# Kernel optimization log

Hardware: AMD Instinct MI355X
Metric: run time of the kernel (lower is better)

The kernel has to match this reference:

```python
import jax, jax.numpy as jnp
import numpy as np

B, D = 64, 65536   # batch, num default boxes
NEG_POS = 3        # negative:positive mining ratio (init arg)


def _bce_with_logits(x, t):
    # numerically stable elementwise BCE-with-logits (matches torch)
    return jnp.maximum(x, 0.0) - x * t + jnp.log1p(jnp.exp(-jnp.abs(x)))


def _smooth_l1(d):
    ad = jnp.abs(d)
    return jnp.where(ad < 1.0, 0.5 * d * d, ad - 0.5)


def setup_inputs() -> dict:
    key = jax.random.key(0)
    k1, k2, k3, k4 = jax.random.split(key, 4)
    loc_data = jax.random.normal(k1, (B, D, 4), dtype=jnp.float32)
    conf_data = jax.random.normal(k2, (B, D, 1), dtype=jnp.float32)
    loc_t = jax.random.normal(k3, (B, D, 4), dtype=jnp.float32)
    conf_t = (jax.random.uniform(k4, (B, D)) < 0.02).astype(jnp.int32)
    return {"loc_data": loc_data, "conf_data": conf_data,
            "loc_t": loc_t, "conf_t": conf_t}


def reference(loc_data, conf_data, loc_t, conf_t):
    pos = conf_t > 0                                  # [B, D]
    num_pos = pos.sum(axis=1, keepdims=True)          # [B, 1]

    # ---- localization loss: smooth-L1 mean over positive box coords ----
    pf = pos[:, :, None].astype(loc_data.dtype)       # [B, D, 1]
    sl1 = _smooth_l1(loc_data - loc_t) * pf           # [B, D, 4]
    n_loc_elems = pf.sum() * 4.0                      # masked-gather -> mean
    loss_l = sl1.sum() / n_loc_elems

    # ---- confidence loss with hard negative mining ----
    logits = conf_data[:, :, 0]                       # [B, D]
    bce = _bce_with_logits(logits, conf_t.astype(logits.dtype))
    bce_neg = jnp.where(pos, 0.0, bce)                # zero-out positives
    # double argsort -> per-row rank of each element's loss (descending)
    loss_idx = jnp.argsort(-bce_neg, axis=1)          # [B, D]
    idx_rank = jnp.argsort(loss_idx, axis=1)          # [B, D]
    num_neg = jnp.minimum(num_pos * NEG_POS, D)       # [B, 1]
    neg = idx_rank < num_neg                          # top-k hardest negatives
    sel = (pos | neg).astype(logits.dtype)            # [B, D]
    loss_c = (bce * sel).sum() / sel.sum()            # mean over selected

    N = num_pos.sum().astype(logits.dtype)
    return (loss_l / N, loss_c / N)
```

## Files before the change

kernel.cpp:

```cpp
#include <hip/hip_runtime.h>
#include <stdint.h>


#define B_ 64
#define D_ 65536
#define NEGPOS 3
#define BPR 16
#define NBLK (B_ * BPR)
#define CHUNK (D_ / BPR)
#define XC 1.25f
#define LCAP 8192
#define HBINS 4096
#define XRANGE 5.0f
#define CJCAP 1024

#define OFF_SL1P     0
#define OFF_BCEP     8192
#define OFF_NP       16384
#define OFF_CC       20480
#define OFF_NEGSUM   24576
#define OFF_KSEL     25088
#define OFF_CAND     32768

__device__ __forceinline__ float softplus_f(float x) {
    return fmaxf(x, 0.0f) + log1pf(expf(-fabsf(x)));
}

__device__ __forceinline__ int bin_of_x(float x) {
    int b = (int)((x - XC) * ((float)HBINS / XRANGE));
    return max(0, min(HBINS - 1, b));
}

__device__ __forceinline__ float smooth_l1_4(float4 a, float4 b) {
    float s = 0.0f, d, ad;
    d = a.x - b.x; ad = fabsf(d); s += (ad < 1.0f) ? 0.5f * d * d : ad - 0.5f;
    d = a.y - b.y; ad = fabsf(d); s += (ad < 1.0f) ? 0.5f * d * d : ad - 0.5f;
    d = a.z - b.z; ad = fabsf(d); s += (ad < 1.0f) ? 0.5f * d * d : ad - 0.5f;
    d = a.w - b.w; ad = fabsf(d); s += (ad < 1.0f) ? 0.5f * d * d : ad - 0.5f;
    return s;
}

__device__ __forceinline__ double wredD(double v) {
#pragma unroll
    for (int o = 32; o > 0; o >>= 1) v += __shfl_down(v, o, 64);
    return v;
}
__device__ __forceinline__ int wredI(int v) {
#pragma unroll
    for (int o = 32; o > 0; o >>= 1) v += __shfl_down(v, o, 64);
    return v;
}

__global__ void __launch_bounds__(256)
mbl_k1(const float4* __restrict__ loc4, const float* __restrict__ conf,
       const float4* __restrict__ loct4, const int* __restrict__ conft,
       unsigned char* __restrict__ ws)
{
    __shared__ float lcand[CHUNK];
    __shared__ unsigned short lpos[CHUNK];
    __shared__ unsigned wtot[4];
    __shared__ double wr[8];

    const int block = blockIdx.x;
    const int base = block * CHUNK;
    const float4* c4 = (const float4*)(conf + base);
    const int4*   t4 = (const int4*)(conft + base);
    const int lane = threadIdx.x & 63, wid = threadIdx.x >> 6;

    float4 xv[4]; int4 tv[4];
#pragma unroll
    for (int it = 0; it < 4; it++) {
        const int g = threadIdx.x + it * 256;
        xv[it] = c4[g];
        tv[it] = t4[g];
    }

    double bcep = 0.0;
    unsigned cntc = 0, cntp = 0;
#pragma unroll
    for (int it = 0; it < 4; it++) {
#pragma unroll
        for (int c = 0; c < 4; c++) {
            float x = (c == 0) ? xv[it].x : (c == 1) ? xv[it].y : (c == 2) ? xv[it].z : xv[it].w;
            int   t = (c == 0) ? tv[it].x : (c == 1) ? tv[it].y : (c == 2) ? tv[it].z : tv[it].w;
            if (t > 0) { cntp++; bcep += (double)(softplus_f(x) - x); }
            else if (x >= XC) cntc++;
        }
    }

    unsigned pk = (cntc << 16) | cntp;
    unsigned incl = pk;
#pragma unroll
    for (int o = 1; o < 64; o <<= 1) {
        unsigned v = __shfl_up(incl, o, 64);
        if (lane >= o) incl += v;
    }
    unsigned excl = incl - pk;
    if (lane == 63) wtot[wid] = incl;
    __syncthreads();
    unsigned wbase = 0;
    for (int w = 0; w < wid; w++) wbase += wtot[w];
    const unsigned tot = wtot[0] + wtot[1] + wtot[2] + wtot[3];
    const unsigned totc = tot >> 16, totp = tot & 0xFFFFu;
    unsigned offc = (excl >> 16) + (wbase >> 16);
    unsigned offp = (excl & 0xFFFFu) + (wbase & 0xFFFFu);

#pragma unroll
    for (int it = 0; it < 4; it++) {
#pragma unroll
        for (int c = 0; c < 4; c++) {
            float x = (c == 0) ? xv[it].x : (c == 1) ? xv[it].y : (c == 2) ? xv[it].z : xv[it].w;
            int   t = (c == 0) ? tv[it].x : (c == 1) ? tv[it].y : (c == 2) ? tv[it].z : tv[it].w;
            const int li = (threadIdx.x + it * 256) * 4 + c;
            if (t > 0) lpos[offp++] = (unsigned short)li;
            else if (x >= XC) lcand[offc++] = x;
        }
    }
    __syncthreads();

    float* seg = (float*)(ws + OFF_CAND) + (size_t)block * CHUNK;
    for (unsigned i = threadIdx.x; i < totc; i += 256) seg[i] = lcand[i];

    double sl1 = 0.0;
    for (unsigned i = threadIdx.x; i < totp; i += 256) {
        const int e = base + (int)lpos[i];
        sl1 += (double)smooth_l1_4(loc4[e], loct4[e]);
    }

    double s1 = wredD(sl1), s2 = wredD(bcep);
    if (lane == 0) { wr[wid] = s1; wr[4 + wid] = s2; }
    __syncthreads();
    if (threadIdx.x == 0) {
        ((double*)(ws + OFF_SL1P))[block] = wr[0] + wr[1] + wr[2] + wr[3];
        ((double*)(ws + OFF_BCEP))[block] = wr[4] + wr[5] + wr[6] + wr[7];
        ((unsigned*)(ws + OFF_NP))[block] = totp;
        ((unsigned*)(ws + OFF_CC))[block] = totc;
    }
}

__device__ __forceinline__ int blockSumI(int v, int* sh) {
    int w = wredI(v);
    const int lane = threadIdx.x & 63, wid = threadIdx.x >> 6;
    __syncthreads();
    if (lane == 0) sh[wid] = w;
    __syncthreads();
    return sh[0] + sh[1] + sh[2] + sh[3];
}

__global__ void __launch_bounds__(256)
mbl_ksel(const float* __restrict__ conf, const int* __restrict__ conft,
         unsigned char* __restrict__ ws)
{
    __shared__ float lval[LCAP];
    __shared__ unsigned hist[HBINS];
    __shared__ unsigned part[256];
    __shared__ unsigned ubuf[CJCAP];
    __shared__ unsigned segoff[BPR + 1];
    __shared__ unsigned scc[BPR];
    __shared__ unsigned wsuf[4];
    __shared__ unsigned shJ, shRemJ, shCj, shNP;
    __shared__ float shXT;
    __shared__ int shI[4];
    __shared__ double wr[4];

    const int row = blockIdx.x;
    const unsigned* cc = (const unsigned*)(ws + OFF_CC) + row * BPR;
    const unsigned* npb = (const unsigned*)(ws + OFF_NP) + row * BPR;
    const int lane = threadIdx.x & 63, wid = threadIdx.x >> 6;

    if (wid == 0) {
        unsigned c = (lane < BPR) ? cc[lane] : 0u;
        unsigned p = (lane < BPR) ? npb[lane] : 0u;
        unsigned inc = c;
#pragma unroll
        for (int o = 1; o < BPR; o <<= 1) {
            unsigned v = __shfl_up(inc, o, 64);
            if (lane >= o) inc += v;
        }
        unsigned ptot = p;
#pragma unroll
        for (int o = 1; o < BPR; o <<= 1) ptot += __shfl_down(ptot, o, 64);
        if (lane < BPR) { segoff[lane] = inc - c; scc[lane] = c; }
        if (lane == BPR - 1) segoff[BPR] = inc;
        if (lane == 0) { shNP = ptot; shCj = 0; }
    }
    __syncthreads();

    const int np = (int)shNP;
    const unsigned n = segoff[BPR];
    long long k = (long long)np * NEGPOS;
    if (k > D_) k = D_;
    long long negs = (long long)D_ - np;
    if (k > negs) k = negs;
    if (threadIdx.x == 0) ((int*)(ws + OFF_KSEL))[row] = (int)k;
    if (k <= 0) {
        if (threadIdx.x == 0) ((double*)(ws + OFF_NEGSUM))[row] = 0.0;
        return;
    }

    const float* cand = (const float*)(ws + OFF_CAND);
    const float* rowc = conf + row * D_;
    const int*   rowt = conft + row * D_;
    const bool fb = ((long long)n < k) || (n > (unsigned)LCAP);
    float xT;
    int rem;

    if (!fb) {
        {
            const int s = threadIdx.x >> 4, li = threadIdx.x & 15;
            const float* gseg = cand + (size_t)(row * BPR + s) * CHUNK;
            const unsigned cs = scc[s], d0 = segoff[s];
            for (unsigned i = li; i < cs; i += 16) lval[d0 + i] = gseg[i];
        }
        for (int i = threadIdx.x; i < HBINS; i += 256) hist[i] = 0;
        __syncthreads();
        for (unsigned i = threadIdx.x; i < n; i += 256)
            atomicAdd(&hist[bin_of_x(lval[i])], 1u);
        __syncthreads();

        {
            unsigned s = 0; const int b0 = threadIdx.x * 16;
#pragma unroll
            for (int i = 0; i < 16; i++) s += hist[b0 + i];
            part[threadIdx.x] = s;
            unsigned suf = s;
#pragma unroll
            for (int o = 1; o < 64; o <<= 1) {
                unsigned v = __shfl_down(suf, o, 64);
                if (lane + o < 64) suf += v;
            }
            if (lane == 0) wsuf[wid] = suf;
            __syncthreads();
            unsigned add = 0;
            for (int w = wid + 1; w < 4; w++) add += wsuf[w];
            suf += add;
            const unsigned sufx = suf - s;
            if ((long long)sufx < k && (long long)suf >= k) {
                long long cum = sufx;
                for (int b = threadIdx.x * 16 + 15; b >= threadIdx.x * 16; b--) {
                    cum += hist[b];
                    if (cum >= k) {
                        shJ = (unsigned)b;
                        shRemJ = (unsigned)(k - (cum - (long long)hist[b]));
                        break;
                    }
                }
            }
        }
        __syncthreads();
        const unsigned J = shJ, remJ = shRemJ;

        for (unsigned i = threadIdx.x; i < n; i += 256) {
            float x = lval[i];
            if ((unsigned)bin_of_x(x) == J) {
                unsigned p = atomicAdd(&shCj, 1u);
                if (p < CJCAP) ubuf[p] = __float_as_uint(x);
            }
        }
        __syncthreads();
        const unsigned cj = shCj;

        if (cj <= CJCAP) {
            for (unsigned i = threadIdx.x; i < cj; i += 256) {
                const float xi = __uint_as_float(ubuf[i]);
                unsigned gt = 0, ge = 0;
                for (unsigned l = 0; l < cj; l++) {
                    const float xl = __uint_as_float(ubuf[l]);
                    gt += (xl > xi) ? 1u : 0u;
                    ge += (xl >= xi) ? 1u : 0u;
                }
                if (gt < remJ && ge >= remJ) shXT = xi;
            }
            __syncthreads();
            xT = shXT;
        } else {
            float flo = XC - 1.0f, fhi = XC + XRANGE + 1.0f;
            for (int it = 0; it < 40; it++) {
                const float mid = 0.5f * (flo + fhi);
                int c = 0;
                for (unsigned i = threadIdx.x; i < n; i += 256)
                    if (lval[i] > mid) c++;
                const int tot = blockSumI(c, shI);
                if ((long long)tot >= k) flo = mid; else fhi = mid;
                if (!(flo < fhi)) break;
            }
            xT = fhi;
        }

        int c = 0;
        double acc = 0.0;
        for (unsigned i = threadIdx.x; i < n; i += 256) {
            float x = lval[i];
            if (x > xT) { c++; acc += (double)softplus_f(x); }
        }
        const int tot = blockSumI(c, shI);
        rem = (int)(k - (long long)tot);
        double t = wredD(acc);
        if (lane == 0) wr[wid] = t;
        __syncthreads();
        if (threadIdx.x == 0)
            ((double*)(ws + OFF_NEGSUM))[row] =
                wr[0] + wr[1] + wr[2] + wr[3] +
                (double)rem * (double)softplus_f(xT);
    } else {
        unsigned lo = 0u, hi = 0xFFFFFFFFu;
        for (int it = 0; it < 32; it++) {
            const unsigned mid = lo + ((hi - lo) >> 1);
            unsigned um = (mid & 0x80000000u) ? (mid & 0x7FFFFFFFu) : ~mid;
            float fm = __uint_as_float(um);
            int c = 0;
            for (int i = threadIdx.x; i < D_; i += 256)
                if (rowt[i] <= 0 && rowc[i] > fm) c++;
            const int tot = blockSumI(c, shI);
            if ((long long)tot >= k) lo = mid; else hi = mid;
        }
        unsigned uT = (hi & 0x80000000u) ? (hi & 0x7FFFFFFFu) : ~hi;
        xT = __uint_as_float(uT);
        int c = 0;
        double acc = 0.0;
        for (int i = threadIdx.x; i < D_; i += 256) {
            if (rowt[i] <= 0) {
                float x = rowc[i];
                if (x > xT) { c++; acc += (double)softplus_f(x); }
            }
        }
        rem = (int)(k - (long long)blockSumI(c, shI));
        double t = wredD(acc);
        if (lane == 0) wr[wid] = t;
        __syncthreads();
        if (threadIdx.x == 0)
            ((double*)(ws + OFF_NEGSUM))[row] =
                wr[0] + wr[1] + wr[2] + wr[3] +
                (double)rem * (double)softplus_f(xT);
    }
}

__global__ void __launch_bounds__(256)
mbl_k5(unsigned char* __restrict__ ws, float* __restrict__ out)
{
    __shared__ double wrA[4], wrB[4], wrC[4];
    __shared__ int shN[4], shK[4];
    const double* sl1p = (const double*)(ws + OFF_SL1P);
    const double* bcep = (const double*)(ws + OFF_BCEP);
    const unsigned* npb = (const unsigned*)(ws + OFF_NP);
    const int* ksel = (const int*)(ws + OFF_KSEL);
    const double* ns = (const double*)(ws + OFF_NEGSUM);

    double a = 0.0, b = 0.0, c = 0.0;
    int n = 0, kk = 0;
    for (int i = threadIdx.x; i < NBLK; i += 256) {
        a += sl1p[i]; b += bcep[i]; n += (int)npb[i];
    }
    if (threadIdx.x < 64) { kk = ksel[threadIdx.x]; c = ns[threadIdx.x]; }

    double ra = wredD(a), rb = wredD(b), rc = wredD(c);
    int rn = wredI(n), rk = wredI(kk);
    const int lane = threadIdx.x & 63, wid = threadIdx.x >> 6;
    if (lane == 0) { wrA[wid] = ra; wrB[wid] = rb; wrC[wid] = rc; shN[wid] = rn; shK[wid] = rk; }
    __syncthreads();
    if (threadIdx.x == 0) {
        double SL1 = wrA[0] + wrA[1] + wrA[2] + wrA[3];
        double BCE = wrB[0] + wrB[1] + wrB[2] + wrB[3];
        double NSUM = wrC[0] + wrC[1] + wrC[2] + wrC[3];
        double Np = (double)(shN[0] + shN[1] + shN[2] + shN[3]);
        double Kt = (double)(shK[0] + shK[1] + shK[2] + shK[3]);
        double out0 = (Np > 0.0) ? (SL1 / (4.0 * Np)) / Np : 0.0;
        double denom = Np + Kt;
        double out1 = (Np > 0.0 && denom > 0.0) ? ((BCE + NSUM) / denom) / Np : 0.0;
        out[0] = (float)out0;
        out[1] = (float)out1;
    }
}

extern "C" void kernel_launch(void* const* d_in, const int* in_sizes, int n_in,
                              void* d_out, int out_size, void* d_ws, size_t ws_size,
                              hipStream_t stream)
{
    const float4* loc4  = (const float4*)d_in[0];
    const float*  conf  = (const float*)d_in[1];
    const float4* loct4 = (const float4*)d_in[2];
    const int*    conft = (const int*)d_in[3];
    unsigned char* ws = (unsigned char*)d_ws;
    float* out = (float*)d_out;

    mbl_k1<<<dim3(NBLK), dim3(256), 0, stream>>>(loc4, conf, loct4, conft, ws);
    mbl_ksel<<<dim3(B_), dim3(256), 0, stream>>>(conf, conft, ws);
    mbl_k5<<<dim3(1), dim3(256), 0, stream>>>(ws, out);
}
```

Baseline: 175.5 us.

## Fuse three kernels into one using last-block-done atomic counters

Merges the per-chunk scan kernel, the per-row hard-negative selection kernel and the final reduction kernel into a single launch. The last block to finish each row, detected through an agent-scope atomic counter, performs that row's selection, and the last row to finish writes the final outputs. Selection now reads candidates straight from global memory instead of staging them in shared memory, and it sums the top-k softplus values directly instead of first locating an exact threshold. This removes two launches and the gaps between them, at the cost of an added memset launch, a serialized tail inside the fused kernel, and a larger shared-memory footprint from the union.

```diff
diff --git a/kernel.cpp b/kernel.cpp
--- a/kernel.cpp
+++ b/kernel.cpp
@@ -9,7 +9,6 @@
 #define NBLK (B_ * BPR)
 #define CHUNK (D_ / BPR)
 #define XC 1.25f
-#define LCAP 8192
 #define HBINS 4096
 #define XRANGE 5.0f
 #define CJCAP 1024
@@ -20,6 +19,7 @@
 #define OFF_CC       20480
 #define OFF_NEGSUM   24576
 #define OFF_KSEL     25088
+#define OFF_CNT      25344
 #define OFF_CAND     32768
 
 __device__ __forceinline__ float softplus_f(float x) {
@@ -51,93 +51,6 @@
     return v;
 }
 
-__global__ void __launch_bounds__(256)
-mbl_k1(const float4* __restrict__ loc4, const float* __restrict__ conf,
-       const float4* __restrict__ loct4, const int* __restrict__ conft,
-       unsigned char* __restrict__ ws)
-{
-    __shared__ float lcand[CHUNK];
-    __shared__ unsigned short lpos[CHUNK];
-    __shared__ unsigned wtot[4];
-    __shared__ double wr[8];
-
-    const int block = blockIdx.x;
-    const int base = block * CHUNK;
-    const float4* c4 = (const float4*)(conf + base);
-    const int4*   t4 = (const int4*)(conft + base);
-    const int lane = threadIdx.x & 63, wid = threadIdx.x >> 6;
-
-    float4 xv[4]; int4 tv[4];
-#pragma unroll
-    for (int it = 0; it < 4; it++) {
-        const int g = threadIdx.x + it * 256;
-        xv[it] = c4[g];
-        tv[it] = t4[g];
-    }
-
-    double bcep = 0.0;
-    unsigned cntc = 0, cntp = 0;
-#pragma unroll
-    for (int it = 0; it < 4; it++) {
-#pragma unroll
-        for (int c = 0; c < 4; c++) {
-            float x = (c == 0) ? xv[it].x : (c == 1) ? xv[it].y : (c == 2) ? xv[it].z : xv[it].w;
-            int   t = (c == 0) ? tv[it].x : (c == 1) ? tv[it].y : (c == 2) ? tv[it].z : tv[it].w;
-            if (t > 0) { cntp++; bcep += (double)(softplus_f(x) - x); }
-            else if (x >= XC) cntc++;
-        }
-    }
-
-    unsigned pk = (cntc << 16) | cntp;
-    unsigned incl = pk;
-#pragma unroll
-    for (int o = 1; o < 64; o <<= 1) {
-        unsigned v = __shfl_up(incl, o, 64);
-        if (lane >= o) incl += v;
-    }
-    unsigned excl = incl - pk;
-    if (lane == 63) wtot[wid] = incl;
-    __syncthreads();
-    unsigned wbase = 0;
-    for (int w = 0; w < wid; w++) wbase += wtot[w];
-    const unsigned tot = wtot[0] + wtot[1] + wtot[2] + wtot[3];
-    const unsigned totc = tot >> 16, totp = tot & 0xFFFFu;
-    unsigned offc = (excl >> 16) + (wbase >> 16);
-    unsigned offp = (excl & 0xFFFFu) + (wbase & 0xFFFFu);
-
-#pragma unroll
-    for (int it = 0; it < 4; it++) {
-#pragma unroll
-        for (int c = 0; c < 4; c++) {
-            float x = (c == 0) ? xv[it].x : (c == 1) ? xv[it].y : (c == 2) ? xv[it].z : xv[it].w;
-            int   t = (c == 0) ? tv[it].x : (c == 1) ? tv[it].y : (c == 2) ? tv[it].z : tv[it].w;
-            const int li = (threadIdx.x + it * 256) * 4 + c;
-            if (t > 0) lpos[offp++] = (unsigned short)li;
-            else if (x >= XC) lcand[offc++] = x;
-        }
-    }
-    __syncthreads();
-
-    float* seg = (float*)(ws + OFF_CAND) + (size_t)block * CHUNK;
-    for (unsigned i = threadIdx.x; i < totc; i += 256) seg[i] = lcand[i];
-
-    double sl1 = 0.0;
-    for (unsigned i = threadIdx.x; i < totp; i += 256) {
-        const int e = base + (int)lpos[i];
-        sl1 += (double)smooth_l1_4(loc4[e], loct4[e]);
-    }
-
-    double s1 = wredD(sl1), s2 = wredD(bcep);
-    if (lane == 0) { wr[wid] = s1; wr[4 + wid] = s2; }
-    __syncthreads();
-    if (threadIdx.x == 0) {
-        ((double*)(ws + OFF_SL1P))[block] = wr[0] + wr[1] + wr[2] + wr[3];
-        ((double*)(ws + OFF_BCEP))[block] = wr[4] + wr[5] + wr[6] + wr[7];
-        ((unsigned*)(ws + OFF_NP))[block] = totp;
-        ((unsigned*)(ws + OFF_CC))[block] = totc;
-    }
-}
-
 __device__ __forceinline__ int blockSumI(int v, int* sh) {
     int w = wredI(v);
     const int lane = threadIdx.x & 63, wid = threadIdx.x >> 6;
@@ -148,29 +61,119 @@
 }
 
 __global__ void __launch_bounds__(256)
-mbl_ksel(const float* __restrict__ conf, const int* __restrict__ conft,
-         unsigned char* __restrict__ ws)
+mbl_fused(const float4* __restrict__ loc4, const float* __restrict__ conf,
+          const float4* __restrict__ loct4, const int* __restrict__ conft,
+          unsigned char* __restrict__ ws, float* __restrict__ out)
 {
-    __shared__ float lval[LCAP];
-    __shared__ unsigned hist[HBINS];
-    __shared__ unsigned part[256];
-    __shared__ unsigned ubuf[CJCAP];
-    __shared__ unsigned segoff[BPR + 1];
-    __shared__ unsigned scc[BPR];
-    __shared__ unsigned wsuf[4];
+    __shared__ union {
+        struct { float lcand[CHUNK]; unsigned short lpos[CHUNK]; } a;
+        struct { unsigned hist[HBINS]; float ubuf[CJCAP]; } b;
+    } u;
+    __shared__ unsigned wtot[4];
+    __shared__ double wr[8];
+    __shared__ double wrC[4];
+    __shared__ int shN[4], shK[4];
+    __shared__ unsigned segoff[BPR + 1], sccS[BPR], wsuf[4];
     __shared__ unsigned shJ, shRemJ, shCj, shNP;
-    __shared__ float shXT;
     __shared__ int shI[4];
-    __shared__ double wr[4];
-
-    const int row = blockIdx.x;
-    const unsigned* cc = (const unsigned*)(ws + OFF_CC) + row * BPR;
-    const unsigned* npb = (const unsigned*)(ws + OFF_NP) + row * BPR;
+    __shared__ int shLast;
+
+    const int block = blockIdx.x;
+    const int row = block >> 4;
+    const int base = block * CHUNK;
     const int lane = threadIdx.x & 63, wid = threadIdx.x >> 6;
 
+    {
+        const float4* c4 = (const float4*)(conf + base);
+        const int4*   t4 = (const int4*)(conft + base);
+
+        float4 xv[4]; int4 tv[4];
+#pragma unroll
+        for (int it = 0; it < 4; it++) {
+            const int g = threadIdx.x + it * 256;
+            xv[it] = c4[g];
+            tv[it] = t4[g];
+        }
+
+        double bcp = 0.0;
+        unsigned cntc = 0, cntp = 0;
+#pragma unroll
+        for (int it = 0; it < 4; it++) {
+#pragma unroll
+            for (int c = 0; c < 4; c++) {
+                float x = (c == 0) ? xv[it].x : (c == 1) ? xv[it].y : (c == 2) ? xv[it].z : xv[it].w;
+                int   t = (c == 0) ? tv[it].x : (c == 1) ? tv[it].y : (c == 2) ? tv[it].z : tv[it].w;
+                if (t > 0) { cntp++; bcp += (double)(softplus_f(x) - x); }
+                else if (x >= XC) cntc++;
+            }
+        }
+
+        unsigned pk = (cntc << 16) | cntp;
+        unsigned incl = pk;
+#pragma unroll
+        for (int o = 1; o < 64; o <<= 1) {
+            unsigned v = __shfl_up(incl, o, 64);
+            if (lane >= o) incl += v;
+        }
+        unsigned excl = incl - pk;
+        if (lane == 63) wtot[wid] = incl;
+        __syncthreads();
+        unsigned wbase = 0;
+        for (int w = 0; w < wid; w++) wbase += wtot[w];
+        const unsigned tot = wtot[0] + wtot[1] + wtot[2] + wtot[3];
+        const unsigned totc = tot >> 16, totp = tot & 0xFFFFu;
+        unsigned offc = (excl >> 16) + (wbase >> 16);
+        unsigned offp = (excl & 0xFFFFu) + (wbase & 0xFFFFu);
+
+#pragma unroll
+        for (int it = 0; it < 4; it++) {
+#pragma unroll
+            for (int c = 0; c < 4; c++) {
+                float x = (c == 0) ? xv[it].x : (c == 1) ? xv[it].y : (c == 2) ? xv[it].z : xv[it].w;
+                int   t = (c == 0) ? tv[it].x : (c == 1) ? tv[it].y : (c == 2) ? tv[it].z : tv[it].w;
+                const int li = (threadIdx.x + it * 256) * 4 + c;
+                if (t > 0) u.a.lpos[offp++] = (unsigned short)li;
+                else if (x >= XC) u.a.lcand[offc++] = x;
+            }
+        }
+        __syncthreads();
+
+        float* seg = (float*)(ws + OFF_CAND) + (size_t)block * CHUNK;
+        for (unsigned i = threadIdx.x; i < totc; i += 256) seg[i] = u.a.lcand[i];
+
+        double sl1 = 0.0;
+        for (unsigned i = threadIdx.x; i < totp; i += 256) {
+            const int e = base + (int)u.a.lpos[i];
+            sl1 += (double)smooth_l1_4(loc4[e], loct4[e]);
+        }
+
+        double s1 = wredD(sl1), s2 = wredD(bcp);
+        if (lane == 0) { wr[wid] = s1; wr[4 + wid] = s2; }
+        __syncthreads();
+        if (threadIdx.x == 0) {
+            ((double*)(ws + OFF_SL1P))[block] = wr[0] + wr[1] + wr[2] + wr[3];
+            ((double*)(ws + OFF_BCEP))[block] = wr[4] + wr[5] + wr[6] + wr[7];
+            ((unsigned*)(ws + OFF_NP))[block] = totp;
+            ((unsigned*)(ws + OFF_CC))[block] = totc;
+        }
+    }
+
+    __syncthreads();
+    if (threadIdx.x == 0) {
+        unsigned old = __hip_atomic_fetch_add(
+            (unsigned*)(ws + OFF_CNT) + row, 1u,
+            __ATOMIC_ACQ_REL, __HIP_MEMORY_SCOPE_AGENT);
+        shLast = (old == BPR - 1) ? 1 : 0;
+    }
+    __syncthreads();
+    if (!shLast) return;
+
+    const unsigned* ccp = (const unsigned*)(ws + OFF_CC) + row * BPR;
+    const unsigned* npp = (const unsigned*)(ws + OFF_NP) + row * BPR;
+
     if (wid == 0) {
-        unsigned c = (lane < BPR) ? cc[lane] : 0u;
-        unsigned p = (lane < BPR) ? npb[lane] : 0u;
+        unsigned c = (lane < BPR) ? ccp[lane] : 0u;
+        unsigned p = (lane < BPR) ? npp[lane] : 0u;
         unsigned inc = c;
 #pragma unroll
         for (int o = 1; o < BPR; o <<= 1) {
@@ -180,7 +183,7 @@
         unsigned ptot = p;
 #pragma unroll
         for (int o = 1; o < BPR; o <<= 1) ptot += __shfl_down(ptot, o, 64);
-        if (lane < BPR) { segoff[lane] = inc - c; scc[lane] = c; }
+        if (lane < BPR) { segoff[lane] = inc - c; sccS[lane] = c; }
         if (lane == BPR - 1) segoff[BPR] = inc;
         if (lane == 0) { shNP = ptot; shCj = 0; }
     }
@@ -193,37 +196,33 @@
     long long negs = (long long)D_ - np;
     if (k > negs) k = negs;
     if (threadIdx.x == 0) ((int*)(ws + OFF_KSEL))[row] = (int)k;
+
+    bool donesum = false;
+    bool needfb = false;
     if (k <= 0) {
         if (threadIdx.x == 0) ((double*)(ws + OFF_NEGSUM))[row] = 0.0;
-        return;
+        donesum = true;
+    } else if ((long long)n < k) {
+        needfb = true;
     }
 
     const float* cand = (const float*)(ws + OFF_CAND);
-    const float* rowc = conf + row * D_;
-    const int*   rowt = conft + row * D_;
-    const bool fb = ((long long)n < k) || (n > (unsigned)LCAP);
-    float xT;
-    int rem;
-
-    if (!fb) {
+
+    if (!donesum && !needfb) {
+        for (int i = threadIdx.x; i < HBINS; i += 256) u.b.hist[i] = 0;
+        __syncthreads();
+        const int s = threadIdx.x >> 4, li = threadIdx.x & 15;
+        const float* gseg = cand + (size_t)(row * BPR + s) * CHUNK;
+        const unsigned cs = sccS[s];
+        for (unsigned i = li; i < cs; i += 16)
+            atomicAdd(&u.b.hist[bin_of_x(gseg[i])], 1u);
+        __syncthreads();
+
         {
-            const int s = threadIdx.x >> 4, li = threadIdx.x & 15;
-            const float* gseg = cand + (size_t)(row * BPR + s) * CHUNK;
-            const unsigned cs = scc[s], d0 = segoff[s];
-            for (unsigned i = li; i < cs; i += 16) lval[d0 + i] = gseg[i];
-        }
-        for (int i = threadIdx.x; i < HBINS; i += 256) hist[i] = 0;
-        __syncthreads();
-        for (unsigned i = threadIdx.x; i < n; i += 256)
-            atomicAdd(&hist[bin_of_x(lval[i])], 1u);
-        __syncthreads();
-
-        {
-            unsigned s = 0; const int b0 = threadIdx.x * 16;
-#pragma unroll
-            for (int i = 0; i < 16; i++) s += hist[b0 + i];
-            part[threadIdx.x] = s;
-            unsigned suf = s;
+            unsigned s16 = 0; const int b0 = threadIdx.x * 16;
+#pragma unroll
+            for (int i = 0; i < 16; i++) s16 += u.b.hist[b0 + i];
+            unsigned suf = s16;
 #pragma unroll
             for (int o = 1; o < 64; o <<= 1) {
                 unsigned v = __shfl_down(suf, o, 64);
@@ -234,14 +233,14 @@
             unsigned add = 0;
             for (int w = wid + 1; w < 4; w++) add += wsuf[w];
             suf += add;
-            const unsigned sufx = suf - s;
+            const unsigned sufx = suf - s16;
             if ((long long)sufx < k && (long long)suf >= k) {
                 long long cum = sufx;
-                for (int b = threadIdx.x * 16 + 15; b >= threadIdx.x * 16; b--) {
-                    cum += hist[b];
+                for (int b = b0 + 15; b >= b0; b--) {
+                    cum += u.b.hist[b];
                     if (cum >= k) {
                         shJ = (unsigned)b;
-                        shRemJ = (unsigned)(k - (cum - (long long)hist[b]));
+                        shRemJ = (unsigned)(k - (cum - (long long)u.b.hist[b]));
                         break;
                     }
                 }
@@ -250,11 +249,14 @@
         __syncthreads();
         const unsigned J = shJ, remJ = shRemJ;
 
-        for (unsigned i = threadIdx.x; i < n; i += 256) {
-            float x = lval[i];
-            if ((unsigned)bin_of_x(x) == J) {
+        double acc = 0.0;
+        for (unsigned i = li; i < cs; i += 16) {
+            const float x = gseg[i];
+            const int b = bin_of_x(x);
+            if (b > (int)J) acc += (double)softplus_f(x);
+            else if (b == (int)J) {
                 unsigned p = atomicAdd(&shCj, 1u);
-                if (p < CJCAP) ubuf[p] = __float_as_uint(x);
+                if (p < CJCAP) u.b.ubuf[p] = x;
             }
         }
         __syncthreads();
@@ -262,47 +264,28 @@
 
         if (cj <= CJCAP) {
             for (unsigned i = threadIdx.x; i < cj; i += 256) {
-                const float xi = __uint_as_float(ubuf[i]);
-                unsigned gt = 0, ge = 0;
+                const float xi = u.b.ubuf[i];
+                unsigned r = 0;
                 for (unsigned l = 0; l < cj; l++) {
-                    const float xl = __uint_as_float(ubuf[l]);
-                    gt += (xl > xi) ? 1u : 0u;
-                    ge += (xl >= xi) ? 1u : 0u;
+                    const float xl = u.b.ubuf[l];
+                    r += (xl > xi || (xl == xi && l < i)) ? 1u : 0u;
                 }
-                if (gt < remJ && ge >= remJ) shXT = xi;
-            }
+                if (r < remJ) acc += (double)softplus_f(xi);
+            }
+            double t = wredD(acc);
+            if (lane == 0) wr[wid] = t;
             __syncthreads();
-            xT = shXT;
+            if (threadIdx.x == 0)
+                ((double*)(ws + OFF_NEGSUM))[row] = wr[0] + wr[1] + wr[2] + wr[3];
+            donesum = true;
         } else {
-            float flo = XC - 1.0f, fhi = XC + XRANGE + 1.0f;
-            for (int it = 0; it < 40; it++) {
-                const float mid = 0.5f * (flo + fhi);
-                int c = 0;
-                for (unsigned i = threadIdx.x; i < n; i += 256)
-                    if (lval[i] > mid) c++;
-                const int tot = blockSumI(c, shI);
-                if ((long long)tot >= k) flo = mid; else fhi = mid;
-                if (!(flo < fhi)) break;
-            }
-            xT = fhi;
-        }
-
-        int c = 0;
-        double acc = 0.0;
-        for (unsigned i = threadIdx.x; i < n; i += 256) {
-            float x = lval[i];
-            if (x > xT) { c++; acc += (double)softplus_f(x); }
-        }
-        const int tot = blockSumI(c, shI);
-        rem = (int)(k - (long long)tot);
-        double t = wredD(acc);
-        if (lane == 0) wr[wid] = t;
-        __syncthreads();
-        if (threadIdx.x == 0)
-            ((double*)(ws + OFF_NEGSUM))[row] =
-                wr[0] + wr[1] + wr[2] + wr[3] +
-                (double)rem * (double)softplus_f(xT);
-    } else {
+            needfb = true;
+        }
+    }
+
+    if (!donesum && needfb) {
+        const float* rowc = conf + row * D_;
+        const int*   rowt = conft + row * D_;
         unsigned lo = 0u, hi = 0xFFFFFFFFu;
         for (int it = 0; it < 32; it++) {
             const unsigned mid = lo + ((hi - lo) >> 1);
@@ -315,7 +298,7 @@
             if ((long long)tot >= k) lo = mid; else hi = mid;
         }
         unsigned uT = (hi & 0x80000000u) ? (hi & 0x7FFFFFFFu) : ~hi;
-        xT = __uint_as_float(uT);
+        float xT = __uint_as_float(uT);
         int c = 0;
         double acc = 0.0;
         for (int i = threadIdx.x; i < D_; i += 256) {
@@ -324,7 +307,7 @@
                 if (x > xT) { c++; acc += (double)softplus_f(x); }
             }
         }
-        rem = (int)(k - (long long)blockSumI(c, shI));
+        int rem = (int)(k - (long long)blockSumI(c, shI));
         double t = wredD(acc);
         if (lane == 0) wr[wid] = t;
         __syncthreads();
@@ -333,42 +316,47 @@
                 wr[0] + wr[1] + wr[2] + wr[3] +
                 (double)rem * (double)softplus_f(xT);
     }
-}
-
-__global__ void __launch_bounds__(256)
-mbl_k5(unsigned char* __restrict__ ws, float* __restrict__ out)
-{
-    __shared__ double wrA[4], wrB[4], wrC[4];
-    __shared__ int shN[4], shK[4];
-    const double* sl1p = (const double*)(ws + OFF_SL1P);
-    const double* bcep = (const double*)(ws + OFF_BCEP);
-    const unsigned* npb = (const unsigned*)(ws + OFF_NP);
-    const int* ksel = (const int*)(ws + OFF_KSEL);
-    const double* ns = (const double*)(ws + OFF_NEGSUM);
-
-    double a = 0.0, b = 0.0, c = 0.0;
-    int n = 0, kk = 0;
-    for (int i = threadIdx.x; i < NBLK; i += 256) {
-        a += sl1p[i]; b += bcep[i]; n += (int)npb[i];
-    }
-    if (threadIdx.x < 64) { kk = ksel[threadIdx.x]; c = ns[threadIdx.x]; }
-
-    double ra = wredD(a), rb = wredD(b), rc = wredD(c);
-    int rn = wredI(n), rk = wredI(kk);
-    const int lane = threadIdx.x & 63, wid = threadIdx.x >> 6;
-    if (lane == 0) { wrA[wid] = ra; wrB[wid] = rb; wrC[wid] = rc; shN[wid] = rn; shK[wid] = rk; }
+
     __syncthreads();
     if (threadIdx.x == 0) {
-        double SL1 = wrA[0] + wrA[1] + wrA[2] + wrA[3];
-        double BCE = wrB[0] + wrB[1] + wrB[2] + wrB[3];
-        double NSUM = wrC[0] + wrC[1] + wrC[2] + wrC[3];
-        double Np = (double)(shN[0] + shN[1] + shN[2] + shN[3]);
-        double Kt = (double)(shK[0] + shK[1] + shK[2] + shK[3]);
-        double out0 = (Np > 0.0) ? (SL1 / (4.0 * Np)) / Np : 0.0;
-        double denom = Np + Kt;
-        double out1 = (Np > 0.0 && denom > 0.0) ? ((BCE + NSUM) / denom) / Np : 0.0;
-        out[0] = (float)out0;
-        out[1] = (float)out1;
+        unsigned old = __hip_atomic_fetch_add(
+            (unsigned*)(ws + OFF_CNT) + B_, 1u,
+            __ATOMIC_ACQ_REL, __HIP_MEMORY_SCOPE_AGENT);
+        shLast = (old == B_ - 1) ? 1 : 0;
+    }
+    __syncthreads();
+    if (!shLast) return;
+
+    {
+        const double* sl1p = (const double*)(ws + OFF_SL1P);
+        const double* bcep = (const double*)(ws + OFF_BCEP);
+        const unsigned* npb = (const unsigned*)(ws + OFF_NP);
+        const int* kselp = (const int*)(ws + OFF_KSEL);
+        const double* nsp = (const double*)(ws + OFF_NEGSUM);
+
+        double a = 0.0, b2 = 0.0, c2 = 0.0;
+        int nn = 0, kk = 0;
+        for (int i = threadIdx.x; i < NBLK; i += 256) {
+            a += sl1p[i]; b2 += bcep[i]; nn += (int)npb[i];
+        }
+        if (threadIdx.x < B_) { kk = kselp[threadIdx.x]; c2 = nsp[threadIdx.x]; }
+
+        double ra = wredD(a), rb = wredD(b2), rc = wredD(c2);
+        int rn = wredI(nn), rk = wredI(kk);
+        if (lane == 0) { wr[wid] = ra; wr[4 + wid] = rb; wrC[wid] = rc; shN[wid] = rn; shK[wid] = rk; }
+        __syncthreads();
+        if (threadIdx.x == 0) {
+            double SL1 = wr[0] + wr[1] + wr[2] + wr[3];
+            double BCE = wr[4] + wr[5] + wr[6] + wr[7];
+            double NSUM = wrC[0] + wrC[1] + wrC[2] + wrC[3];
+            double Np = (double)(shN[0] + shN[1] + shN[2] + shN[3]);
+            double Kt = (double)(shK[0] + shK[1] + shK[2] + shK[3]);
+            double out0 = (Np > 0.0) ? (SL1 / (4.0 * Np)) / Np : 0.0;
+            double denom = Np + Kt;
+            double out1 = (Np > 0.0 && denom > 0.0) ? ((BCE + NSUM) / denom) / Np : 0.0;
+            out[0] = (float)out0;
+            out[1] = (float)out1;
+        }
     }
 }
 
@@ -383,7 +371,6 @@
     unsigned char* ws = (unsigned char*)d_ws;
     float* out = (float*)d_out;
 
-    mbl_k1<<<dim3(NBLK), dim3(256), 0, stream>>>(loc4, conf, loct4, conft, ws);
-    mbl_ksel<<<dim3(B_), dim3(256), 0, stream>>>(conf, conft, ws);
-    mbl_k5<<<dim3(1), dim3(256), 0, stream>>>(ws, out);
-}
+    hipMemsetAsync(ws + OFF_CNT, 0, (B_ + 1) * sizeof(unsigned), stream);
+    mbl_fused<<<dim3(NBLK), dim3(256), 0, stream>>>(loc4, conf, loct4, conft, ws, out);
+}
```

New measurement: 232.2 us. 32.3% more time.

## Stream candidates from global segments in selection kernel, drop LDS staging and threshold pass

Applied to the files above, without the earlier changes.

The per-row selection kernel no longer copies all candidate logits into a large shared buffer. It builds the histogram by reading each segment directly with float4 loads. The boundary bin is now resolved in one fused pass that sums softplus for bins above the threshold and collects the boundary-bin values. Those values get an exact tie-broken rank, so the separate threshold search and recount passes go away. This cuts shared-memory use, which may raise occupancy, and removes the LCAP-overflow fallback. The cost is reading the candidates from global memory twice, and an overflowing boundary bin now falls back to the full-row bisection.

```diff
diff --git a/kernel.cpp b/kernel.cpp
--- a/kernel.cpp
+++ b/kernel.cpp
@@ -9,18 +9,17 @@
 #define NBLK (B_ * BPR)
 #define CHUNK (D_ / BPR)
 #define XC 1.25f
-#define LCAP 8192
 #define HBINS 4096
 #define XRANGE 5.0f
 #define CJCAP 1024
 
-#define OFF_SL1P     0
-#define OFF_BCEP     8192
-#define OFF_NP       16384
-#define OFF_CC       20480
-#define OFF_NEGSUM   24576
-#define OFF_KSEL     25088
-#define OFF_CAND     32768
+#define OFF_SL1P   0
+#define OFF_BCEP   8192
+#define OFF_NP     16384
+#define OFF_CC     20480
+#define OFF_NEGSUM 24576
+#define OFF_KSEL   25088
+#define OFF_CAND   32768
 
 __device__ __forceinline__ float softplus_f(float x) {
     return fmaxf(x, 0.0f) + log1pf(expf(-fabsf(x)));
@@ -49,6 +48,15 @@
 #pragma unroll
     for (int o = 32; o > 0; o >>= 1) v += __shfl_down(v, o, 64);
     return v;
+}
+
+__device__ __forceinline__ int blockSumI(int v, int* sh) {
+    int w = wredI(v);
+    const int lane = threadIdx.x & 63, wid = threadIdx.x >> 6;
+    __syncthreads();
+    if (lane == 0) sh[wid] = w;
+    __syncthreads();
+    return sh[0] + sh[1] + sh[2] + sh[3];
 }
 
 __global__ void __launch_bounds__(256)
@@ -59,13 +67,14 @@
     __shared__ float lcand[CHUNK];
     __shared__ unsigned short lpos[CHUNK];
     __shared__ unsigned wtot[4];
-    __shared__ double wr[8];
+    __shared__ double wrD[8];
 
     const int block = blockIdx.x;
     const int base = block * CHUNK;
+    const int lane = threadIdx.x & 63, wid = threadIdx.x >> 6;
+
     const float4* c4 = (const float4*)(conf + base);
     const int4*   t4 = (const int4*)(conft + base);
-    const int lane = threadIdx.x & 63, wid = threadIdx.x >> 6;
 
     float4 xv[4]; int4 tv[4];
 #pragma unroll
@@ -75,7 +84,7 @@
         tv[it] = t4[g];
     }
 
-    double bcep = 0.0;
+    double bcp = 0.0;
     unsigned cntc = 0, cntp = 0;
 #pragma unroll
     for (int it = 0; it < 4; it++) {
@@ -83,7 +92,7 @@
         for (int c = 0; c < 4; c++) {
             float x = (c == 0) ? xv[it].x : (c == 1) ? xv[it].y : (c == 2) ? xv[it].z : xv[it].w;
             int   t = (c == 0) ? tv[it].x : (c == 1) ? tv[it].y : (c == 2) ? tv[it].z : tv[it].w;
-            if (t > 0) { cntp++; bcep += (double)(softplus_f(x) - x); }
+            if (t > 0) { cntp++; bcp += (double)(softplus_f(x) - x); }
             else if (x >= XC) cntc++;
         }
     }
@@ -127,182 +136,153 @@
         sl1 += (double)smooth_l1_4(loc4[e], loct4[e]);
     }
 
-    double s1 = wredD(sl1), s2 = wredD(bcep);
-    if (lane == 0) { wr[wid] = s1; wr[4 + wid] = s2; }
+    double s1 = wredD(sl1), s2 = wredD(bcp);
+    if (lane == 0) { wrD[wid] = s1; wrD[4 + wid] = s2; }
     __syncthreads();
     if (threadIdx.x == 0) {
-        ((double*)(ws + OFF_SL1P))[block] = wr[0] + wr[1] + wr[2] + wr[3];
-        ((double*)(ws + OFF_BCEP))[block] = wr[4] + wr[5] + wr[6] + wr[7];
+        ((double*)(ws + OFF_SL1P))[block] = wrD[0] + wrD[1] + wrD[2] + wrD[3];
+        ((double*)(ws + OFF_BCEP))[block] = wrD[4] + wrD[5] + wrD[6] + wrD[7];
         ((unsigned*)(ws + OFF_NP))[block] = totp;
         ((unsigned*)(ws + OFF_CC))[block] = totc;
     }
 }
 
-__device__ __forceinline__ int blockSumI(int v, int* sh) {
-    int w = wredI(v);
+__global__ void __launch_bounds__(256)
+mbl_k2(const float* __restrict__ conf, const int* __restrict__ conft,
+       unsigned char* __restrict__ ws)
+{
+    __shared__ unsigned hist[HBINS];
+    __shared__ float ubuf[CJCAP];
+    __shared__ unsigned wsuf[4], sccS[BPR];
+    __shared__ double wrD[4];
+    __shared__ int shI[4];
+    __shared__ unsigned shJ, shRemJ, shNP, shT, shCj;
+
+    const int row = blockIdx.x;
     const int lane = threadIdx.x & 63, wid = threadIdx.x >> 6;
-    __syncthreads();
-    if (lane == 0) sh[wid] = w;
-    __syncthreads();
-    return sh[0] + sh[1] + sh[2] + sh[3];
-}
-
-__global__ void __launch_bounds__(256)
-mbl_ksel(const float* __restrict__ conf, const int* __restrict__ conft,
-         unsigned char* __restrict__ ws)
-{
-    __shared__ float lval[LCAP];
-    __shared__ unsigned hist[HBINS];
-    __shared__ unsigned part[256];
-    __shared__ unsigned ubuf[CJCAP];
-    __shared__ unsigned segoff[BPR + 1];
-    __shared__ unsigned scc[BPR];
-    __shared__ unsigned wsuf[4];
-    __shared__ unsigned shJ, shRemJ, shCj, shNP;
-    __shared__ float shXT;
-    __shared__ int shI[4];
-    __shared__ double wr[4];
-
-    const int row = blockIdx.x;
-    const unsigned* cc = (const unsigned*)(ws + OFF_CC) + row * BPR;
-    const unsigned* npb = (const unsigned*)(ws + OFF_NP) + row * BPR;
-    const int lane = threadIdx.x & 63, wid = threadIdx.x >> 6;
 
     if (wid == 0) {
-        unsigned c = (lane < BPR) ? cc[lane] : 0u;
-        unsigned p = (lane < BPR) ? npb[lane] : 0u;
-        unsigned inc = c;
+        const unsigned* ccp = (const unsigned*)(ws + OFF_CC) + row * BPR;
+        const unsigned* npp = (const unsigned*)(ws + OFF_NP) + row * BPR;
+        unsigned c = (lane < BPR) ? ccp[lane] : 0u;
+        unsigned p = (lane < BPR) ? npp[lane] : 0u;
+        if (lane < BPR) sccS[lane] = c;
+        unsigned ct = c, pt = p;
 #pragma unroll
         for (int o = 1; o < BPR; o <<= 1) {
-            unsigned v = __shfl_up(inc, o, 64);
-            if (lane >= o) inc += v;
-        }
-        unsigned ptot = p;
-#pragma unroll
-        for (int o = 1; o < BPR; o <<= 1) ptot += __shfl_down(ptot, o, 64);
-        if (lane < BPR) { segoff[lane] = inc - c; scc[lane] = c; }
-        if (lane == BPR - 1) segoff[BPR] = inc;
-        if (lane == 0) { shNP = ptot; shCj = 0; }
+            ct += __shfl_down(ct, o, 64);
+            pt += __shfl_down(pt, o, 64);
+        }
+        if (lane == 0) { shT = ct; shNP = pt; shCj = 0; }
     }
     __syncthreads();
 
     const int np = (int)shNP;
-    const unsigned n = segoff[BPR];
+    const unsigned n = shT;
     long long k = (long long)np * NEGPOS;
     if (k > D_) k = D_;
     long long negs = (long long)D_ - np;
     if (k > negs) k = negs;
     if (threadIdx.x == 0) ((int*)(ws + OFF_KSEL))[row] = (int)k;
+
+    bool done = false, fb = false;
     if (k <= 0) {
         if (threadIdx.x == 0) ((double*)(ws + OFF_NEGSUM))[row] = 0.0;
-        return;
-    }
-
-    const float* cand = (const float*)(ws + OFF_CAND);
-    const float* rowc = conf + row * D_;
-    const int*   rowt = conft + row * D_;
-    const bool fb = ((long long)n < k) || (n > (unsigned)LCAP);
-    float xT;
-    int rem;
-
-    if (!fb) {
-        {
-            const int s = threadIdx.x >> 4, li = threadIdx.x & 15;
-            const float* gseg = cand + (size_t)(row * BPR + s) * CHUNK;
-            const unsigned cs = scc[s], d0 = segoff[s];
-            for (unsigned i = li; i < cs; i += 16) lval[d0 + i] = gseg[i];
-        }
+        done = true;
+    } else if ((long long)n < k) {
+        fb = true;
+    }
+
+    if (!done && !fb) {
+        const int s = threadIdx.x >> 4, li = threadIdx.x & 15;
+        const unsigned cs = sccS[s];
+        const float4* seg4 = (const float4*)((const float*)(ws + OFF_CAND)
+                             + (size_t)(row * BPR + s) * CHUNK);
+
         for (int i = threadIdx.x; i < HBINS; i += 256) hist[i] = 0;
         __syncthreads();
-        for (unsigned i = threadIdx.x; i < n; i += 256)
-            atomicAdd(&hist[bin_of_x(lval[i])], 1u);
-        __syncthreads();
-
-        {
-            unsigned s = 0; const int b0 = threadIdx.x * 16;
-#pragma unroll
-            for (int i = 0; i < 16; i++) s += hist[b0 + i];
-            part[threadIdx.x] = s;
-            unsigned suf = s;
-#pragma unroll
-            for (int o = 1; o < 64; o <<= 1) {
-                unsigned v = __shfl_down(suf, o, 64);
-                if (lane + o < 64) suf += v;
+
+        for (unsigned i0 = (unsigned)li * 4u; i0 < cs; i0 += 64u) {
+            const float4 q = seg4[i0 >> 2];
+            if (i0 + 0 < cs) atomicAdd(&hist[bin_of_x(q.x)], 1u);
+            if (i0 + 1 < cs) atomicAdd(&hist[bin_of_x(q.y)], 1u);
+            if (i0 + 2 < cs) atomicAdd(&hist[bin_of_x(q.z)], 1u);
+            if (i0 + 3 < cs) atomicAdd(&hist[bin_of_x(q.w)], 1u);
+        }
+        __syncthreads();
+
+        unsigned s16 = 0;
+        const int b0i = threadIdx.x * 16;
+#pragma unroll
+        for (int j = 0; j < 16; j++) s16 += hist[b0i + j];
+        unsigned suf = s16;
+#pragma unroll
+        for (int o = 1; o < 64; o <<= 1) {
+            unsigned v = __shfl_down(suf, o, 64);
+            if (lane + o < 64) suf += v;
+        }
+        if (lane == 0) wsuf[wid] = suf;
+        __syncthreads();
+        unsigned addw = 0;
+        for (int w = wid + 1; w < 4; w++) addw += wsuf[w];
+        suf += addw;
+        const unsigned sufx = suf - s16;
+        if ((long long)sufx < k && (long long)suf >= k) {
+            long long cum = sufx;
+            for (int j = 15; j >= 0; j--) {
+                cum += hist[b0i + j];
+                if (cum >= k) {
+                    shJ = (unsigned)(b0i + j);
+                    shRemJ = (unsigned)(k - (cum - (long long)hist[b0i + j]));
+                    break;
+                }
             }
-            if (lane == 0) wsuf[wid] = suf;
-            __syncthreads();
-            unsigned add = 0;
-            for (int w = wid + 1; w < 4; w++) add += wsuf[w];
-            suf += add;
-            const unsigned sufx = suf - s;
-            if ((long long)sufx < k && (long long)suf >= k) {
-                long long cum = sufx;
-                for (int b = threadIdx.x * 16 + 15; b >= threadIdx.x * 16; b--) {
-                    cum += hist[b];
-                    if (cum >= k) {
-                        shJ = (unsigned)b;
-                        shRemJ = (unsigned)(k - (cum - (long long)hist[b]));
-                        break;
+        }
+        __syncthreads();
+        const unsigned J = shJ, remJ = shRemJ;
+
+        double acc = 0.0;
+        for (unsigned i0 = (unsigned)li * 4u; i0 < cs; i0 += 64u) {
+            const float4 q = seg4[i0 >> 2];
+#pragma unroll
+            for (int c = 0; c < 4; c++) {
+                if (i0 + (unsigned)c < cs) {
+                    const float x = (c == 0) ? q.x : (c == 1) ? q.y : (c == 2) ? q.z : q.w;
+                    const int b = bin_of_x(x);
+                    if (b > (int)J) acc += (double)softplus_f(x);
+                    else if (b == (int)J) {
+                        unsigned sl = atomicAdd(&shCj, 1u);
+                        if (sl < CJCAP) ubuf[sl] = x;
                     }
                 }
             }
         }
         __syncthreads();
-        const unsigned J = shJ, remJ = shRemJ;
-
-        for (unsigned i = threadIdx.x; i < n; i += 256) {
-            float x = lval[i];
-            if ((unsigned)bin_of_x(x) == J) {
-                unsigned p = atomicAdd(&shCj, 1u);
-                if (p < CJCAP) ubuf[p] = __float_as_uint(x);
-            }
-        }
-        __syncthreads();
         const unsigned cj = shCj;
 
         if (cj <= CJCAP) {
             for (unsigned i = threadIdx.x; i < cj; i += 256) {
-                const float xi = __uint_as_float(ubuf[i]);
-                unsigned gt = 0, ge = 0;
+                const float xi = ubuf[i];
+                unsigned r = 0;
                 for (unsigned l = 0; l < cj; l++) {
-                    const float xl = __uint_as_float(ubuf[l]);
-                    gt += (xl > xi) ? 1u : 0u;
-                    ge += (xl >= xi) ? 1u : 0u;
+                    const float xl = ubuf[l];
+                    r += (xl > xi || (xl == xi && l < i)) ? 1u : 0u;
                 }
-                if (gt < remJ && ge >= remJ) shXT = xi;
+                if (r < remJ) acc += (double)softplus_f(xi);
             }
+            double t = wredD(acc);
+            if (lane == 0) wrD[wid] = t;
             __syncthreads();
-            xT = shXT;
-        } else {
-            float flo = XC - 1.0f, fhi = XC + XRANGE + 1.0f;
-            for (int it = 0; it < 40; it++) {
-                const float mid = 0.5f * (flo + fhi);
-                int c = 0;
-                for (unsigned i = threadIdx.x; i < n; i += 256)
-                    if (lval[i] > mid) c++;
-                const int tot = blockSumI(c, shI);
-                if ((long long)tot >= k) flo = mid; else fhi = mid;
-                if (!(flo < fhi)) break;
-            }
-            xT = fhi;
-        }
-
-        int c = 0;
-        double acc = 0.0;
-        for (unsigned i = threadIdx.x; i < n; i += 256) {
-            float x = lval[i];
-            if (x > xT) { c++; acc += (double)softplus_f(x); }
-        }
-        const int tot = blockSumI(c, shI);
-        rem = (int)(k - (long long)tot);
-        double t = wredD(acc);
-        if (lane == 0) wr[wid] = t;
-        __syncthreads();
-        if (threadIdx.x == 0)
-            ((double*)(ws + OFF_NEGSUM))[row] =
-                wr[0] + wr[1] + wr[2] + wr[3] +
-                (double)rem * (double)softplus_f(xT);
-    } else {
+            if (threadIdx.x == 0)
+                ((double*)(ws + OFF_NEGSUM))[row] =
+                    wrD[0] + wrD[1] + wrD[2] + wrD[3];
+            done = true;
+        } else fb = true;
+    }
+
+    if (!done && fb) {
+        const float* rowc = conf + row * D_;
+        const int*   rowt = conft + row * D_;
         unsigned lo = 0u, hi = 0xFFFFFFFFu;
         for (int it = 0; it < 32; it++) {
             const unsigned mid = lo + ((hi - lo) >> 1);
@@ -315,7 +295,7 @@
             if ((long long)tot >= k) lo = mid; else hi = mid;
         }
         unsigned uT = (hi & 0x80000000u) ? (hi & 0x7FFFFFFFu) : ~hi;
-        xT = __uint_as_float(uT);
+        float xT = __uint_as_float(uT);
         int c = 0;
         double acc = 0.0;
         for (int i = threadIdx.x; i < D_; i += 256) {
@@ -324,13 +304,13 @@
                 if (x > xT) { c++; acc += (double)softplus_f(x); }
             }
         }
-        rem = (int)(k - (long long)blockSumI(c, shI));
+        int rem = (int)(k - (long long)blockSumI(c, shI));
         double t = wredD(acc);
-        if (lane == 0) wr[wid] = t;
+        if (lane == 0) wrD[wid] = t;
         __syncthreads();
         if (threadIdx.x == 0)
             ((double*)(ws + OFF_NEGSUM))[row] =
-                wr[0] + wr[1] + wr[2] + wr[3] +
+                wrD[0] + wrD[1] + wrD[2] + wrD[3] +
                 (double)rem * (double)softplus_f(xT);
     }
 }
@@ -351,7 +331,7 @@
     for (int i = threadIdx.x; i < NBLK; i += 256) {
         a += sl1p[i]; b += bcep[i]; n += (int)npb[i];
     }
-    if (threadIdx.x < 64) { kk = ksel[threadIdx.x]; c = ns[threadIdx.x]; }
+    if (threadIdx.x < B_) { kk = ksel[threadIdx.x]; c = ns[threadIdx.x]; }
 
     double ra = wredD(a), rb = wredD(b), rc = wredD(c);
     int rn = wredI(n), rk = wredI(kk);
@@ -384,6 +364,6 @@
     float* out = (float*)d_out;
 
     mbl_k1<<<dim3(NBLK), dim3(256), 0, stream>>>(loc4, conf, loct4, conft, ws);
-    mbl_ksel<<<dim3(B_), dim3(256), 0, stream>>>(conf, conft, ws);
+    mbl_k2<<<dim3(B_), dim3(256), 0, stream>>>(conf, conft, ws);
     mbl_k5<<<dim3(1), dim3(256), 0, stream>>>(ws, out);
 }
```

Measured after the change: 174.7 us. Within noise of the previous version (-0.5%).
